# Kernel optimization log

Hardware: AMD Instinct MI355X
Metric: run time of the kernel (lower is better)

Reference implementation:

```python
import jax, jax.numpy as jnp
import numpy as np

B, F, T, K = 16, 256, 1024, 10


def setup_inputs() -> dict:
    key = jax.random.key(0)
    k1, k2, k3, k4, k5 = jax.random.split(key, 5)
    mu = jax.random.normal(k1, (B, F, T, K), dtype=jnp.float32)
    log_std = jax.random.normal(k2, (B, F, T, K), dtype=jnp.float32)
    pi_logits = jax.random.normal(k3, (B, F, T, K), dtype=jnp.float32)
    u_cat = jax.random.uniform(k4, (B, F, T), dtype=jnp.float32)
    eps = jax.random.normal(k5, (B, F, T), dtype=jnp.float32)
    return {"mu": mu, "log_std": log_std, "pi_logits": pi_logits,
            "u_cat": u_cat, "eps": eps}


def reference(mu, log_std, pi_logits, u_cat, eps):
    # GMM per-pixel sampling (sample_gmm_batch):
    #   pi  = softmax(pi_logits)                  mixture weights
    #   k   = categorical(pi) via inverse-CDF using uniform u_cat
    #   out = mu[k] + exp(log_std[k]) * eps       reparameterized normal draw
    pi = jax.nn.softmax(pi_logits, axis=-1)              # [B,F,T,K]
    cdf = jnp.cumsum(pi, axis=-1)                        # [B,F,T,K]
    # component index: number of cdf entries strictly below u
    k_idx = jnp.sum(cdf < u_cat[..., None], axis=-1)     # [B,F,T]
    k_idx = jnp.clip(k_idx, 0, K - 1)
    mu_k = jnp.take_along_axis(mu, k_idx[..., None], axis=-1)[..., 0]
    ls_k = jnp.take_along_axis(log_std, k_idx[..., None], axis=-1)[..., 0]
    out = mu_k + jnp.exp(ls_k) * eps                     # [B,F,T]
    return out
```

## Files before the change

kernel.cpp:

```cpp
#include <hip/hip_runtime.h>
#include <math.h>


#define KMIX 10

__device__ __forceinline__ int compute_k(const float* lt, float uval) {
    float m = lt[0];
    #pragma unroll
    for (int j = 1; j < KMIX; ++j) m = fmaxf(m, lt[j]);

    float e[KMIX];
    float S = 0.f;
    #pragma unroll
    for (int j = 0; j < KMIX; ++j) {
        e[j] = expf(lt[j] - m);
        S += e[j];
    }

    float cdf = 0.f;
    int k = 0;
    #pragma unroll
    for (int j = 0; j < KMIX; ++j) {
        cdf += e[j] / S;
        k += (cdf < uval) ? 1 : 0;
    }
    return (k > KMIX - 1) ? (KMIX - 1) : k;
}

__global__ __launch_bounds__(256) void gmm_sample_kernel(
    const float* __restrict__ mu,
    const float* __restrict__ log_std,
    const float* __restrict__ pi_logits,
    const float* __restrict__ u_cat,
    const float* __restrict__ eps,
    float* __restrict__ out,
    int npairs)
{
    int p = blockIdx.x * blockDim.x + threadIdx.x;
    if (p >= npairs) return;

    size_t base = (size_t)p * (2 * KMIX);

    const float4* pl4 = reinterpret_cast<const float4*>(pi_logits + base);
    float l[2 * KMIX];
    #pragma unroll
    for (int j = 0; j < 5; ++j) {
        float4 a = pl4[j];
        l[4 * j + 0] = a.x; l[4 * j + 1] = a.y;
        l[4 * j + 2] = a.z; l[4 * j + 3] = a.w;
    }
    float2 uu = *reinterpret_cast<const float2*>(u_cat + 2 * (size_t)p);
    float2 ee = *reinterpret_cast<const float2*>(eps + 2 * (size_t)p);

    int k0 = compute_k(l, uu.x);
    int k1 = compute_k(l + KMIX, uu.y);

    size_t i0 = base + (size_t)k0;
    size_t i1 = base + KMIX + (size_t)k1;
    float mk0 = mu[i0];
    float sk0 = log_std[i0];
    float mk1 = mu[i1];
    float sk1 = log_std[i1];

    float2 r;
    r.x = mk0 + expf(sk0) * ee.x;
    r.y = mk1 + expf(sk1) * ee.y;
    *reinterpret_cast<float2*>(out + 2 * (size_t)p) = r;
}

extern "C" void kernel_launch(void* const* d_in, const int* in_sizes, int n_in,
                              void* d_out, int out_size, void* d_ws, size_t ws_size,
                              hipStream_t stream) {
    const float* mu        = (const float*)d_in[0];
    const float* log_std   = (const float*)d_in[1];
    const float* pi_logits = (const float*)d_in[2];
    const float* u_cat     = (const float*)d_in[3];
    const float* eps       = (const float*)d_in[4];
    float* out = (float*)d_out;

    int N = in_sizes[3];
    int npairs = N / 2;
    int block = 256;
    int grid = (npairs + block - 1) / block;
    gmm_sample_kernel<<<grid, block, 0, stream>>>(mu, log_std, pi_logits,
                                                  u_cat, eps, out, npairs);
}
```

Baseline: 449.0 us.

## Stage mixture arrays through shared memory with coalesced loads before gathering

Each block cooperatively loads its slice of pi_logits, mu and log_std with coalesced float4 loads into LDS, then each thread reads its logits and gathers the selected mu/log_std from shared memory. This replaces strided per-thread vector loads and dependent global gathers with fully coalesced streaming. It reads all of mu and log_std unconditionally and uses about 30KB LDS per 128-thread block, limiting occupancy.

```diff
diff --git a/kernel.cpp b/kernel.cpp
--- a/kernel.cpp
+++ b/kernel.cpp
@@ -3,6 +3,10 @@
 
 
 #define KMIX 10
+#define TPB 128
+#define PX_PER_BLOCK (TPB * 2)
+#define F_PER_ARRAY (PX_PER_BLOCK * KMIX)
+#define F4_PER_ARRAY (F_PER_ARRAY / 4)
 
 __device__ __forceinline__ int compute_k(const float* lt, float uval) {
     float m = lt[0];
@@ -27,7 +31,7 @@
     return (k > KMIX - 1) ? (KMIX - 1) : k;
 }
 
-__global__ __launch_bounds__(256) void gmm_sample_kernel(
+__global__ __launch_bounds__(TPB, 2) void gmm_sample_kernel(
     const float* __restrict__ mu,
     const float* __restrict__ log_std,
     const float* __restrict__ pi_logits,
@@ -36,36 +40,62 @@
     float* __restrict__ out,
     int npairs)
 {
-    int p = blockIdx.x * blockDim.x + threadIdx.x;
-    if (p >= npairs) return;
+    __shared__ float4 s_pi4[F4_PER_ARRAY];
+    __shared__ float4 s_mu4[F4_PER_ARRAY];
+    __shared__ float4 s_ls4[F4_PER_ARRAY];
 
-    size_t base = (size_t)p * (2 * KMIX);
+    const int tid = threadIdx.x;
+    const size_t blk = blockIdx.x;
+    const size_t base_f4 = blk * F4_PER_ARRAY;
 
-    const float4* pl4 = reinterpret_cast<const float4*>(pi_logits + base);
+    const float4* gpi = reinterpret_cast<const float4*>(pi_logits) + base_f4;
+    const float4* gmu = reinterpret_cast<const float4*>(mu)        + base_f4;
+    const float4* gls = reinterpret_cast<const float4*>(log_std)   + base_f4;
+
+    float4 t[15];
+    #pragma unroll
+    for (int j = 0; j < 5; ++j) t[j]      = gpi[j * TPB + tid];
+    #pragma unroll
+    for (int j = 0; j < 5; ++j) t[5 + j]  = gmu[j * TPB + tid];
+    #pragma unroll
+    for (int j = 0; j < 5; ++j) t[10 + j] = gls[j * TPB + tid];
+
+    const size_t pair = blk * TPB + tid;
+    float2 uu = reinterpret_cast<const float2*>(u_cat)[pair];
+    float2 ee = reinterpret_cast<const float2*>(eps)[pair];
+
+    #pragma unroll
+    for (int j = 0; j < 5; ++j) s_pi4[j * TPB + tid] = t[j];
+    #pragma unroll
+    for (int j = 0; j < 5; ++j) s_mu4[j * TPB + tid] = t[5 + j];
+    #pragma unroll
+    for (int j = 0; j < 5; ++j) s_ls4[j * TPB + tid] = t[10 + j];
+
+    __syncthreads();
+
     float l[2 * KMIX];
     #pragma unroll
     for (int j = 0; j < 5; ++j) {
-        float4 a = pl4[j];
+        float4 a = s_pi4[tid * 5 + j];
         l[4 * j + 0] = a.x; l[4 * j + 1] = a.y;
         l[4 * j + 2] = a.z; l[4 * j + 3] = a.w;
     }
-    float2 uu = *reinterpret_cast<const float2*>(u_cat + 2 * (size_t)p);
-    float2 ee = *reinterpret_cast<const float2*>(eps + 2 * (size_t)p);
 
     int k0 = compute_k(l, uu.x);
     int k1 = compute_k(l + KMIX, uu.y);
 
-    size_t i0 = base + (size_t)k0;
-    size_t i1 = base + KMIX + (size_t)k1;
-    float mk0 = mu[i0];
-    float sk0 = log_std[i0];
-    float mk1 = mu[i1];
-    float sk1 = log_std[i1];
+    const float* s_mu = reinterpret_cast<const float*>(s_mu4);
+    const float* s_ls = reinterpret_cast<const float*>(s_ls4);
+    float mk0 = s_mu[20 * tid + k0];
+    float sk0 = s_ls[20 * tid + k0];
+    float mk1 = s_mu[20 * tid + KMIX + k1];
+    float sk1 = s_ls[20 * tid + KMIX + k1];
 
     float2 r;
     r.x = mk0 + expf(sk0) * ee.x;
     r.y = mk1 + expf(sk1) * ee.y;
-    *reinterpret_cast<float2*>(out + 2 * (size_t)p) = r;
+    if (pair < (size_t)npairs)
+        reinterpret_cast<float2*>(out)[pair] = r;
 }
 
 extern "C" void kernel_launch(void* const* d_in, const int* in_sizes, int n_in,
@@ -80,8 +110,7 @@
 
     int N = in_sizes[3];
     int npairs = N / 2;
-    int block = 256;
-    int grid = (npairs + block - 1) / block;
-    gmm_sample_kernel<<<grid, block, 0, stream>>>(mu, log_std, pi_logits,
-                                                  u_cat, eps, out, npairs);
+    int grid = (npairs + TPB - 1) / TPB;
+    gmm_sample_kernel<<<grid, TPB, 0, stream>>>(mu, log_std, pi_logits,
+                                                u_cat, eps, out, npairs);
 }
```

Result: no change. 450.5 us (+0.3%).

## Stream tiles into LDS with async double-buffered DMA in a persistent kernel

Applied to the files above, without the earlier changes.

Replaces the one-thread-per-pair kernel with a persistent grid of 512 blocks of 128 threads. Each block walks a contiguous range of tiles, and each tile stages pi_logits, mu, log_std, u and eps through global_load_lds into double-buffered LDS. The next tile is prefetched while the current one is computed, with vmcnt waits and barriers keeping the two in order. Global loads become fully coalesced and overlapped with compute, and the mu/log_std gathers turn into LDS reads. The cost is reading the whole of mu and log_std rather than gathered elements, plus low occupancy from the 64KB LDS footprint per block.

```diff
diff --git a/kernel.cpp b/kernel.cpp
--- a/kernel.cpp
+++ b/kernel.cpp
@@ -3,6 +3,23 @@
 
 
 #define KMIX 10
+#define TPB 128
+#define F4_ARR 640
+#define F4_U 64
+#define F4_TILE 2048
+#define NBLOCKS 512
+
+__device__ __forceinline__ void dma16(const float4* g, float4* l) {
+    __builtin_amdgcn_global_load_lds(
+        (const __attribute__((address_space(1))) void*)g,
+        (__attribute__((address_space(3))) void*)l, 16, 0, 0);
+}
+
+__device__ __forceinline__ void dma4(const float* g, float* l) {
+    __builtin_amdgcn_global_load_lds(
+        (const __attribute__((address_space(1))) void*)g,
+        (__attribute__((address_space(3))) void*)l, 4, 0, 0);
+}
 
 __device__ __forceinline__ int compute_k(const float* lt, float uval) {
     float m = lt[0];
@@ -27,45 +44,107 @@
     return (k > KMIX - 1) ? (KMIX - 1) : k;
 }
 
-__global__ __launch_bounds__(256) void gmm_sample_kernel(
+__device__ __forceinline__ void stage_tile(
+    const float4* __restrict__ gpi, const float4* __restrict__ gmu,
+    const float4* __restrict__ gls, const float* __restrict__ gu,
+    const float* __restrict__ ge, long t, float4* buf, int tid)
+{
+    const float4* p = gpi + t * F4_ARR;
+    const float4* m = gmu + t * F4_ARR;
+    const float4* s = gls + t * F4_ARR;
+    #pragma unroll
+    for (int j = 0; j < 5; ++j) dma16(p + j * TPB + tid, buf + j * TPB + tid);
+    #pragma unroll
+    for (int j = 0; j < 5; ++j) dma16(m + j * TPB + tid, buf + F4_ARR + j * TPB + tid);
+    #pragma unroll
+    for (int j = 0; j < 5; ++j) dma16(s + j * TPB + tid, buf + 2 * F4_ARR + j * TPB + tid);
+
+    const float* u = gu + t * (2 * TPB);
+    const float* e = ge + t * (2 * TPB);
+    float* su = reinterpret_cast<float*>(buf + 3 * F4_ARR);
+    float* se = reinterpret_cast<float*>(buf + 3 * F4_ARR + F4_U);
+    #pragma unroll
+    for (int j = 0; j < 2; ++j) dma4(u + j * TPB + tid, su + j * TPB + tid);
+    #pragma unroll
+    for (int j = 0; j < 2; ++j) dma4(e + j * TPB + tid, se + j * TPB + tid);
+}
+
+__device__ __forceinline__ void compute_tile(const float4* buf, long t,
+                                             float* __restrict__ out, int tid)
+{
+    float l[2 * KMIX];
+    #pragma unroll
+    for (int j = 0; j < 5; ++j) {
+        float4 a = buf[tid * 5 + j];
+        l[4 * j + 0] = a.x; l[4 * j + 1] = a.y;
+        l[4 * j + 2] = a.z; l[4 * j + 3] = a.w;
+    }
+    const float2* su2 = reinterpret_cast<const float2*>(buf + 3 * F4_ARR);
+    const float2* se2 = reinterpret_cast<const float2*>(buf + 3 * F4_ARR + F4_U);
+    float2 uu = su2[tid];
+    float2 ee = se2[tid];
+
+    int k0 = compute_k(l, uu.x);
+    int k1 = compute_k(l + KMIX, uu.y);
+
+    const float* smu = reinterpret_cast<const float*>(buf + F4_ARR);
+    const float* sls = reinterpret_cast<const float*>(buf + 2 * F4_ARR);
+    float mk0 = smu[20 * tid + k0];
+    float sk0 = sls[20 * tid + k0];
+    float mk1 = smu[20 * tid + KMIX + k1];
+    float sk1 = sls[20 * tid + KMIX + k1];
+
+    float2 r;
+    r.x = mk0 + expf(sk0) * ee.x;
+    r.y = mk1 + expf(sk1) * ee.y;
+    reinterpret_cast<float2*>(out)[t * TPB + tid] = r;
+}
+
+__global__ __launch_bounds__(TPB, 1) void gmm_sample_kernel(
     const float* __restrict__ mu,
     const float* __restrict__ log_std,
     const float* __restrict__ pi_logits,
     const float* __restrict__ u_cat,
     const float* __restrict__ eps,
     float* __restrict__ out,
-    int npairs)
+    int ntiles)
 {
-    int p = blockIdx.x * blockDim.x + threadIdx.x;
-    if (p >= npairs) return;
+    __shared__ float4 lds4[2 * F4_TILE];
 
-    size_t base = (size_t)p * (2 * KMIX);
+    const int tid = threadIdx.x;
+    const int tpbk = (ntiles + gridDim.x - 1) / gridDim.x;
+    long t0 = (long)blockIdx.x * tpbk;
+    long tend = t0 + tpbk;
+    if (tend > ntiles) tend = ntiles;
+    if (t0 >= tend) return;
 
-    const float4* pl4 = reinterpret_cast<const float4*>(pi_logits + base);
-    float l[2 * KMIX];
-    #pragma unroll
-    for (int j = 0; j < 5; ++j) {
-        float4 a = pl4[j];
-        l[4 * j + 0] = a.x; l[4 * j + 1] = a.y;
-        l[4 * j + 2] = a.z; l[4 * j + 3] = a.w;
+    const float4* gpi = reinterpret_cast<const float4*>(pi_logits);
+    const float4* gmu = reinterpret_cast<const float4*>(mu);
+    const float4* gls = reinterpret_cast<const float4*>(log_std);
+
+    float4* buf0 = lds4;
+    float4* buf1 = lds4 + F4_TILE;
+
+    stage_tile(gpi, gmu, gls, u_cat, eps, t0, buf0, tid);
+
+    for (long t = t0; t < tend; ++t) {
+        float4* bcur = ((t - t0) & 1) ? buf1 : buf0;
+        float4* bnxt = ((t - t0) & 1) ? buf0 : buf1;
+
+        if (t + 1 < tend) {
+            stage_tile(gpi, gmu, gls, u_cat, eps, t + 1, bnxt, tid);
+            asm volatile("s_waitcnt vmcnt(19)" ::: "memory");
+        } else {
+            asm volatile("s_waitcnt vmcnt(0)" ::: "memory");
+        }
+        __builtin_amdgcn_s_barrier();
+        __builtin_amdgcn_sched_barrier(0);
+
+        compute_tile(bcur, t, out, tid);
+
+        __builtin_amdgcn_sched_barrier(0);
+        __builtin_amdgcn_s_barrier();
     }
-    float2 uu = *reinterpret_cast<const float2*>(u_cat + 2 * (size_t)p);
-    float2 ee = *reinterpret_cast<const float2*>(eps + 2 * (size_t)p);
-
-    int k0 = compute_k(l, uu.x);
-    int k1 = compute_k(l + KMIX, uu.y);
-
-    size_t i0 = base + (size_t)k0;
-    size_t i1 = base + KMIX + (size_t)k1;
-    float mk0 = mu[i0];
-    float sk0 = log_std[i0];
-    float mk1 = mu[i1];
-    float sk1 = log_std[i1];
-
-    float2 r;
-    r.x = mk0 + expf(sk0) * ee.x;
-    r.y = mk1 + expf(sk1) * ee.y;
-    *reinterpret_cast<float2*>(out + 2 * (size_t)p) = r;
 }
 
 extern "C" void kernel_launch(void* const* d_in, const int* in_sizes, int n_in,
@@ -80,8 +159,8 @@
 
     int N = in_sizes[3];
     int npairs = N / 2;
-    int block = 256;
-    int grid = (npairs + block - 1) / block;
-    gmm_sample_kernel<<<grid, block, 0, stream>>>(mu, log_std, pi_logits,
-                                                  u_cat, eps, out, npairs);
+    int ntiles = npairs / TPB;
+    int grid = (ntiles < NBLOCKS) ? ntiles : NBLOCKS;
+    gmm_sample_kernel<<<grid, TPB, 0, stream>>>(mu, log_std, pi_logits,
+                                                u_cat, eps, out, ntiles);
 }
```

Result: slower. 468.5 us (+4.3%).
